# Kernel optimization log

Hardware: AMD Instinct MI355X
Metric: run time of the kernel (lower is better)

## Reference

```python
import jax, jax.numpy as jnp
import numpy as np

N = 30000
F_IN = 500
HID = 16
OUT = 3
E = 960000


def setup_inputs() -> dict:
    key = jax.random.key(0)
    ks = jax.random.split(key, 10)
    x = jax.random.normal(ks[0], (N, F_IN), dtype=jnp.float32)
    edge_index = jax.random.randint(ks[1], (2, E), 0, N, dtype=jnp.int32)
    # CNN params (torch Conv1d: weight [out, in, k], bias [out])
    s1 = 1.0 / np.sqrt(1 * 3)
    s2 = 1.0 / np.sqrt(HID * 3)
    conv1_w = jax.random.uniform(ks[2], (HID, 1, 3), jnp.float32, -s1, s1)
    conv1_b = jax.random.uniform(ks[3], (HID,), jnp.float32, -s1, s1)
    conv2_w = jax.random.uniform(ks[4], (HID, HID, 3), jnp.float32, -s2, s2)
    conv2_b = jax.random.uniform(ks[5], (HID,), jnp.float32, -s2, s2)
    # GCNConv params (glorot weight [in, out], zero bias)
    g1 = np.sqrt(6.0 / (HID + HID))
    g2 = np.sqrt(6.0 / (HID + OUT))
    gcn1_w = jax.random.uniform(ks[6], (HID, HID), jnp.float32, -g1, g1)
    gcn1_b = jnp.zeros((HID,), jnp.float32)
    gcn2_w = jax.random.uniform(ks[7], (HID, OUT), jnp.float32, -g2, g2)
    gcn2_b = jnp.zeros((OUT,), jnp.float32)
    return {"x": x, "conv1_w": conv1_w, "conv1_b": conv1_b,
            "conv2_w": conv2_w, "conv2_b": conv2_b,
            "gcn1_w": gcn1_w, "gcn1_b": gcn1_b,
            "gcn2_w": gcn2_w, "gcn2_b": gcn2_b,
            "edge_index": edge_index}


def _conv1d(x, w, b):
    # x: [N, C_in, L], w: [C_out, C_in, 3], padding=1
    y = jax.lax.conv_general_dilated(
        x, w, window_strides=(1,), padding=[(1, 1)],
        dimension_numbers=("NCH", "OIH", "NCH"))
    return y + b[None, :, None]


def _gcn_conv(x, w, b, src, dst, n):
    # x: [n, d_in] -> [n, d_out]; Kipf normalization with self-loops
    h = x @ w
    loop = jnp.arange(n, dtype=src.dtype)
    s = jnp.concatenate([src, loop])
    d = jnp.concatenate([dst, loop])
    deg = jax.ops.segment_sum(jnp.ones_like(d, dtype=h.dtype), d, num_segments=n)
    dinv = jnp.where(deg > 0, jax.lax.rsqrt(deg), 0.0)
    norm = dinv[s] * dinv[d]                      # [E+n]
    msg = h[s] * norm[:, None]                    # gather + scale
    return jax.ops.segment_sum(msg, d, num_segments=n) + b


def reference(x, conv1_w, conv1_b, conv2_w, conv2_b,
              gcn1_w, gcn1_b, gcn2_w, gcn2_b, edge_index):
    # CNN feature extractor over feature axis
    h = x[:, None, :]                             # [N, 1, F_IN]
    h = jax.nn.relu(_conv1d(h, conv1_w, conv1_b))  # [N, HID, F_IN]
    h = jax.nn.relu(_conv1d(h, conv2_w, conv2_b))  # [N, HID, F_IN]
    h = jnp.max(h, axis=2)                        # global max pool -> [N, HID]
    # GCN
    src, dst = edge_index[0], edge_index[1]
    n = h.shape[0]
    h = jax.nn.relu(_gcn_conv(h, gcn1_w, gcn1_b, src, dst, n))
    h = _gcn_conv(h, gcn2_w, gcn2_b, src, dst, n)  # [N, OUT]
    return jax.nn.log_softmax(h, axis=1)
```

## Files before the change

kernel.cpp:

```cpp
#include <hip/hip_runtime.h>
#include <hip/hip_bf16.h>

#define N_NODES 30000
#define F_INLEN 500
#define HID 16
#define OUTC 3
#define NEDGE 960000
#define YP 16
#define NBIN 938
#define HBLK 128
#define EPRH (NEDGE / HBLK)
#define ECAP 1536

typedef float  f32x4 __attribute__((ext_vector_type(4)));
typedef float  f32x2 __attribute__((ext_vector_type(2)));
typedef short  s16x8 __attribute__((ext_vector_type(8)));

static __device__ __forceinline__ unsigned short f2bf(float f) {
    unsigned int u = __float_as_uint(f);
    unsigned int r = (u + 0x7fffu + ((u >> 16) & 1u)) >> 16;
    return (unsigned short)r;
}
static __device__ __forceinline__ unsigned int pack_bf16x2(float v0, float v1) {
#if __has_builtin(__builtin_amdgcn_cvt_pk_bf16_f32)
    typedef __bf16 bf16x2_t __attribute__((ext_vector_type(2)));
    union { bf16x2_t v; unsigned int u; } cv;
    cv.v = __builtin_amdgcn_cvt_pk_bf16_f32(v0, v1);
    return cv.u;
#else
    return __builtin_amdgcn_perm(__float_as_uint(v1), __float_as_uint(v0), 0x07060302);
#endif
}

__global__ __launch_bounds__(256) void hist_kernel(
    const float* __restrict__ w2, short* __restrict__ bfragsG,
    const int* __restrict__ dst, int* __restrict__ degi, int* __restrict__ cntbase)
{
    const int tid = threadIdx.x;
    if (blockIdx.x == HBLK) {
        if (tid < 64) {
            const int n16 = tid & 15, q = tid >> 4;
#pragma unroll
            for (int j = 0; j < 8; j++) {
                {
                    const int c = q * 8 + j;
                    const int t = c >> 4, i = c & 15;
                    bfragsG[tid * 16 + j] = (short)f2bf(w2[n16 * 48 + i * 3 + t]);
                }
                {
                    const int c = 32 + q * 8 + j;
                    short v = 0;
                    if (c < 48) { const int t = c >> 4, i = c & 15; v = (short)f2bf(w2[n16 * 48 + i * 3 + t]); }
                    bfragsG[tid * 16 + 8 + j] = v;
                }
            }
        }
        return;
    }
    __shared__ int histH[NBIN];
    for (int i = tid; i < NBIN; i += 256) histH[i] = 0;
    __syncthreads();
    const int e0 = blockIdx.x * EPRH;
    for (int e = e0 + tid; e < e0 + EPRH; e += 256) {
        const int d = dst[e];
        atomicAdd(&histH[d >> 5], 1);
        atomicAdd(&degi[d], 1);
    }
    __syncthreads();
    for (int i = tid; i < NBIN; i += 256) cntbase[blockIdx.x * NBIN + i] = histH[i];
}

__global__ __launch_bounds__(256, 8) void conv_reorder(
    const float* __restrict__ x,
    const float* __restrict__ w1, const float* __restrict__ b1,
    const float* __restrict__ b2, const short* __restrict__ bfragsG,
    const int* __restrict__ src, const int* __restrict__ dst,
    const int* __restrict__ degi, const int* __restrict__ cntbase,
    int* __restrict__ packed, int* __restrict__ binstart,
    float* __restrict__ h0)
{
    __shared__ __align__(16) unsigned short yh[516 * YP];
    __shared__ __align__(16) float xp[502];
    __shared__ float red[64];

    const int tid = threadIdx.x;

    if (blockIdx.x < HBLK) {
        int* scA    = (int*)yh;
        int* scB    = scA + NBIN;
        int* totb   = scB + NBIN;
        int* cursor = totb + NBIN;
        const int blk = blockIdx.x;
        for (int bin = tid; bin < NBIN; bin += 256) {
            int tot = 0, psum = 0;
            for (int k = 0; k < HBLK; k++) {
                const int c = cntbase[k * NBIN + bin];
                tot += c;
                if (k < blk) psum += c;
            }
            scA[bin]    = tot;
            totb[bin]   = tot;
            cursor[bin] = psum;
        }
        __syncthreads();
        int* pA = scA; int* pB = scB;
        for (int off = 1; off < NBIN; off <<= 1) {
            for (int i = tid; i < NBIN; i += 256)
                pB[i] = pA[i] + ((i >= off) ? pA[i - off] : 0);
            __syncthreads();
            int* tp = pA; pA = pB; pB = tp;
        }
        for (int i = tid; i < NBIN; i += 256) {
            const int excl = pA[i] - totb[i];
            cursor[i] += excl;
            if (blk == 0) binstart[i] = excl;
        }
        if (blk == 0 && tid == 0) binstart[NBIN] = NEDGE;
        __syncthreads();
        const int e0 = blk * EPRH;
        for (int e = e0 + tid; e < e0 + EPRH; e += 256) {
            const int d = dst[e];
            const int pos = atomicAdd(&cursor[d >> 5], 1);
            packed[pos] = src[e] | (d << 15);
        }
        return;
    }

    const int node = blockIdx.x - HBLK;
    const int dgi  = degi[node];
    const int lane = tid & 63;
    const int wave = tid >> 6;
    const int n16  = lane & 15;
    const int q    = lane >> 4;

    if (tid == 0) { xp[0] = 0.f; xp[501] = 0.f; }
    if (tid < 125) {
        const float4 v = ((const float4*)(x + (long long)node * F_INLEN))[tid];
        xp[4 * tid + 1] = v.x; xp[4 * tid + 2] = v.y;
        xp[4 * tid + 3] = v.z; xp[4 * tid + 4] = v.w;
    }
    {
        const int ri = tid >> 4;
        const int row = (ri == 0) ? 0 : (500 + ri);
        yh[row * YP + (tid & 15)] = 0;
    }
    const s16x8* bfp = (const s16x8*)(bfragsG + lane * 16);
    const s16x8 bh0 = bfp[0], bh1 = bfp[1];

    f32x2 wt0[8], wt1[8], wt2[8], bbv[8];
#pragma unroll
    for (int cp = 0; cp < 8; cp++) {
        const int c0 = 2 * cp, c1 = 2 * cp + 1;
        wt0[cp] = (f32x2){w1[c0 * 3 + 0], w1[c1 * 3 + 0]};
        wt1[cp] = (f32x2){w1[c0 * 3 + 1], w1[c1 * 3 + 1]};
        wt2[cp] = (f32x2){w1[c0 * 3 + 2], w1[c1 * 3 + 2]};
        bbv[cp] = (f32x2){b1[c0], b1[c1]};
    }
    __syncthreads();

    for (int p = tid; p < 500; p += 256) {
        const float x0 = xp[p], x1 = xp[p + 1], x2 = xp[p + 2];
        const f32x2 xv0 = {x0, x0}, xv1 = {x1, x1}, xv2 = {x2, x2};
        const f32x2 zero = {0.f, 0.f};
        unsigned int hp[8];
#pragma unroll
        for (int cp = 0; cp < 8; cp++) {
            f32x2 a = __builtin_elementwise_fma(wt0[cp], xv0, bbv[cp]);
            a = __builtin_elementwise_fma(wt1[cp], xv1, a);
            a = __builtin_elementwise_fma(wt2[cp], xv2, a);
            a = __builtin_elementwise_max(a, zero);
            hp[cp] = pack_bf16x2(a[0], a[1]);
        }
        uint4* d = (uint4*)&yh[(p + 1) * YP];
        d[0] = make_uint4(hp[0], hp[1], hp[2], hp[3]);
        d[1] = make_uint4(hp[4], hp[5], hp[6], hp[7]);
    }
    __syncthreads();

    const unsigned short* ybase = yh + (n16 + (q >> 1)) * YP + (q & 1) * 8
                                     + wave * (8 * 16 * YP);
    f32x4 mxv = {-3.0e38f, -3.0e38f, -3.0e38f, -3.0e38f};
    f32x4 mxt = {-3.0e38f, -3.0e38f, -3.0e38f, -3.0e38f};
#pragma unroll
    for (int it = 0; it < 8; it++) {
        const s16x8 ah0 = *(const s16x8*)(ybase + it * (16 * YP));
        const s16x8 ah1 = *(const s16x8*)(ybase + it * (16 * YP) + 2 * YP);
        f32x4 acc = {0.f, 0.f, 0.f, 0.f};
        acc = __builtin_amdgcn_mfma_f32_16x16x32_bf16(ah0, bh0, acc, 0, 0, 0);
        acc = __builtin_amdgcn_mfma_f32_16x16x32_bf16(ah1, bh1, acc, 0, 0, 0);
        if (it < 7) mxv = __builtin_elementwise_max(mxv, acc);
        else        mxt = __builtin_elementwise_max(mxt, acc);
    }
    if (wave < 3 || q == 0) mxv = __builtin_elementwise_max(mxv, mxt);
    float m = fmaxf(fmaxf(mxv[0], mxv[1]), fmaxf(mxv[2], mxv[3]));
    m = fmaxf(m, __shfl_xor(m, 16));
    m = fmaxf(m, __shfl_xor(m, 32));
    if (lane < 16) red[wave * 16 + lane] = m;
    __syncthreads();
    if (tid < 16) {
        const float mm = fmaxf(fmaxf(red[tid], red[16 + tid]), fmaxf(red[32 + tid], red[48 + tid]));
        const float dv = rsqrtf((float)(dgi + 1));
        h0[node * HID + tid] = fmaxf(mm + b2[tid], 0.f) * dv;
    }
}

__global__ __launch_bounds__(512) void agg1_kernel(
    const int* __restrict__ binstart, int* __restrict__ packed,
    const float* __restrict__ h0, const int* __restrict__ degi,
    const float* __restrict__ W1, const float* __restrict__ b1g,
    const float* __restrict__ W2, float4* __restrict__ t2p4,
    int* __restrict__ binofs)
{
    __shared__ float w1s[256];
    __shared__ float w2s[48];
    __shared__ float b1s[16];
    __shared__ float accS[32 * 17];
    __shared__ int srt[ECAP];
    __shared__ int h32[32], ls32[32], lofs32[32];
    const int tid = threadIdx.x;
    const int blk = blockIdx.x;
    if (tid < 256) w1s[tid] = W1[tid];
    if (tid < 48) w2s[tid] = W2[tid];
    if (tid < 16) b1s[tid] = b1g[tid];
    if (tid < 32) {
        const int nd = blk * 32 + tid;
        const int v = (nd < N_NODES) ? degi[nd] : 0;
        h32[tid] = v;
        int inc = v;
#pragma unroll
        for (int off = 1; off < 32; off <<= 1) {
            const int y = __shfl_up(inc, off);
            if (tid >= off) inc += y;
        }
        ls32[tid] = inc - v;
        lofs32[tid] = inc - v;
    }
    const int beg = binstart[blk];
    const int cnt = binstart[blk + 1] - beg;
    __syncthreads();
    for (int j = tid; j < cnt; j += 512) {
        const int p = packed[beg + j];
        const int pos = atomicAdd(&lofs32[(p >> 15) & 31], 1);
        srt[pos] = p;
    }
    __syncthreads();
    for (int j = tid; j < cnt; j += 512) packed[beg + j] = srt[j];
    if (tid < 32) {
        binofs[blk * 64 + tid]      = ls32[tid];
        binofs[blk * 64 + 32 + tid] = h32[tid];
    }
    const int n = tid >> 4;
    const int eslot = (tid >> 2) & 3;
    const int q = tid & 3;
    const int node = blk * 32 + n;
    const bool valid = node < N_NODES;
    f32x4 acc = {0.f, 0.f, 0.f, 0.f};
    if (valid) {
        const int s0 = ls32[n];
        const int s1 = s0 + h32[n];
        for (int i = s0 + eslot; i < s1; i += 4) {
            const int s = srt[i] & 32767;
            acc += *(const f32x4*)(h0 + s * HID + q * 4);
        }
    }
#pragma unroll
    for (int c = 0; c < 4; c++) {
        acc[c] += __shfl_xor(acc[c], 4);
        acc[c] += __shfl_xor(acc[c], 8);
    }
    if (valid && eslot == 0) {
        acc += *(const f32x4*)(h0 + node * HID + q * 4);
        accS[n * 17 + q * 4 + 0] = acc[0];
        accS[n * 17 + q * 4 + 1] = acc[1];
        accS[n * 17 + q * 4 + 2] = acc[2];
        accS[n * 17 + q * 4 + 3] = acc[3];
    }
    __syncthreads();
    if (tid < 128) {
        const int n2 = tid >> 2;
        const int node2 = blk * 32 + n2;
        if (node2 < N_NODES) {
            const float dv = rsqrtf((float)(h32[n2] + 1));
            const int q2 = tid & 3;
            float y0 = 0.f, y1 = 0.f, y2 = 0.f, y3 = 0.f;
#pragma unroll
            for (int i = 0; i < 16; i++) {
                const float a = accS[n2 * 17 + i];
                y0 = fmaf(a, w1s[i * 16 + q2 * 4 + 0], y0);
                y1 = fmaf(a, w1s[i * 16 + q2 * 4 + 1], y1);
                y2 = fmaf(a, w1s[i * 16 + q2 * 4 + 2], y2);
                y3 = fmaf(a, w1s[i * 16 + q2 * 4 + 3], y3);
            }
            float d0 = 0.f, d1 = 0.f, d2 = 0.f;
            const float yv[4] = {y0, y1, y2, y3};
#pragma unroll
            for (int j = 0; j < 4; j++) {
                const int o = q2 * 4 + j;
                const float h = fmaxf(b1s[o] + dv * yv[j], 0.f);
                d0 = fmaf(h, w2s[o * 3 + 0], d0);
                d1 = fmaf(h, w2s[o * 3 + 1], d1);
                d2 = fmaf(h, w2s[o * 3 + 2], d2);
            }
            d0 += __shfl_xor(d0, 1); d0 += __shfl_xor(d0, 2);
            d1 += __shfl_xor(d1, 1); d1 += __shfl_xor(d1, 2);
            d2 += __shfl_xor(d2, 1); d2 += __shfl_xor(d2, 2);
            if (q2 == 0) t2p4[node2] = make_float4(d0 * dv, d1 * dv, d2 * dv, dv);
        }
    }
}

__global__ __launch_bounds__(512) void agg2_kernel(
    const int* __restrict__ binstart, const int* __restrict__ packed,
    const float4* __restrict__ t2p4, const int* __restrict__ binofs,
    const float* __restrict__ b2g, float* __restrict__ out)
{
    __shared__ int ofs[64];
    const int tid = threadIdx.x;
    const int blk = blockIdx.x;
    const int beg = binstart[blk];
    if (tid < 64) ofs[tid] = binofs[blk * 64 + tid];
    __syncthreads();
    const int n = tid >> 4;
    const int ln16 = tid & 15;
    const int node = blk * 32 + n;
    float a0 = 0.f, a1 = 0.f, a2 = 0.f;
    if (node < N_NODES) {
        const int s0 = ofs[n];
        const int s1 = s0 + ofs[32 + n];
        for (int i = s0 + ln16; i < s1; i += 16) {
            const int s = packed[beg + i] & 32767;
            const float4 v = t2p4[s];
            a0 += v.x; a1 += v.y; a2 += v.z;
        }
    }
#pragma unroll
    for (int msk = 1; msk < 16; msk <<= 1) {
        a0 += __shfl_xor(a0, msk);
        a1 += __shfl_xor(a1, msk);
        a2 += __shfl_xor(a2, msk);
    }
    if (ln16 == 0 && node < N_NODES) {
        const float4 self = t2p4[node];
        const float dv = self.w;
        const float z0 = b2g[0] + dv * (a0 + self.x);
        const float z1 = b2g[1] + dv * (a1 + self.y);
        const float z2 = b2g[2] + dv * (a2 + self.z);
        const float m = fmaxf(z0, fmaxf(z1, z2));
        const float lg = m + logf(expf(z0 - m) + expf(z1 - m) + expf(z2 - m));
        out[node * 3 + 0] = z0 - lg;
        out[node * 3 + 1] = z1 - lg;
        out[node * 3 + 2] = z2 - lg;
    }
}

extern "C" void kernel_launch(void* const* d_in, const int* in_sizes, int n_in,
                              void* d_out, int out_size, void* d_ws, size_t ws_size,
                              hipStream_t stream)
{
    const float* x   = (const float*)d_in[0];
    const float* w1  = (const float*)d_in[1];
    const float* b1  = (const float*)d_in[2];
    const float* w2  = (const float*)d_in[3];
    const float* b2  = (const float*)d_in[4];
    const float* g1w = (const float*)d_in[5];
    const float* g1b = (const float*)d_in[6];
    const float* g2w = (const float*)d_in[7];
    const float* g2b = (const float*)d_in[8];
    const int*   ei  = (const int*)d_in[9];
    const int* src = ei;
    const int* dst = ei + NEDGE;

    float* ws = (float*)d_ws;
    float*  h0      = ws;
    float4* t2p4    = (float4*)(ws + 480000);
    int*    degi    = (int*)(ws + 600000);
    int*    cntbase = (int*)(ws + 630000);
    int*    binstart= (int*)(ws + 750064);
    int*    packed  = (int*)(ws + 751104);
    int*    binofs  = (int*)(ws + 1711104);
    short*  bfragsG = (short*)(ws + 1771136);
    float*  out     = (float*)d_out;

    hipMemsetAsync(degi, 0, N_NODES * sizeof(int), stream);
    hist_kernel<<<HBLK + 1, 256, 0, stream>>>(w2, bfragsG, dst, degi, cntbase);
    conv_reorder<<<HBLK + N_NODES, 256, 0, stream>>>(x, w1, b1, b2, bfragsG,
                                                     src, dst, degi, cntbase,
                                                     packed, binstart, h0);
    agg1_kernel<<<NBIN, 512, 0, stream>>>(binstart, packed, h0, degi,
                                          g1w, g1b, g2w, t2p4, binofs);
    agg2_kernel<<<NBIN, 512, 0, stream>>>(binstart, packed, t2p4, binofs, g2b, out);
}
```

Measured before the change: 214.2 us.

## Replace bin prefix-scan with fixed-capacity bin slots and global atomic cursors

Drops the per-block shared histogram, the cntbase matrix and the 128-way prefix scan that computed exact bin start offsets. Each bin now gets a fixed slot of 1280 entries, filled through a global atomic cursor per bin, and the bin edge count is derived from the degree prefix inside agg1. This removes the scan work and the cntbase traffic but adds global atomic contention on 938 counters. It also assumes no bin ever holds more than 1280 edges, which holds only for roughly uniform random graphs.

```diff
diff --git a/kernel.cpp b/kernel.cpp
--- a/kernel.cpp
+++ b/kernel.cpp
@@ -10,6 +10,7 @@
 #define NBIN 938
 #define HBLK 128
 #define EPRH (NEDGE / HBLK)
+#define ECAPS 1280
 #define ECAP 1536
 
 typedef float  f32x4 __attribute__((ext_vector_type(4)));
@@ -34,7 +35,7 @@
 
 __global__ __launch_bounds__(256) void hist_kernel(
     const float* __restrict__ w2, short* __restrict__ bfragsG,
-    const int* __restrict__ dst, int* __restrict__ degi, int* __restrict__ cntbase)
+    const int* __restrict__ dst, int* __restrict__ degi)
 {
     const int tid = threadIdx.x;
     if (blockIdx.x == HBLK) {
@@ -57,17 +58,10 @@
         }
         return;
     }
-    __shared__ int histH[NBIN];
-    for (int i = tid; i < NBIN; i += 256) histH[i] = 0;
-    __syncthreads();
     const int e0 = blockIdx.x * EPRH;
     for (int e = e0 + tid; e < e0 + EPRH; e += 256) {
-        const int d = dst[e];
-        atomicAdd(&histH[d >> 5], 1);
-        atomicAdd(&degi[d], 1);
-    }
-    __syncthreads();
-    for (int i = tid; i < NBIN; i += 256) cntbase[blockIdx.x * NBIN + i] = histH[i];
+        atomicAdd(&degi[dst[e]], 1);
+    }
 }
 
 __global__ __launch_bounds__(256, 8) void conv_reorder(
@@ -75,9 +69,8 @@
     const float* __restrict__ w1, const float* __restrict__ b1,
     const float* __restrict__ b2, const short* __restrict__ bfragsG,
     const int* __restrict__ src, const int* __restrict__ dst,
-    const int* __restrict__ degi, const int* __restrict__ cntbase,
-    int* __restrict__ packed, int* __restrict__ binstart,
-    float* __restrict__ h0)
+    const int* __restrict__ degi, int* __restrict__ bincur,
+    int* __restrict__ packed, float* __restrict__ h0)
 {
     __shared__ __align__(16) unsigned short yh[516 * YP];
     __shared__ __align__(16) float xp[502];
@@ -86,42 +79,12 @@
     const int tid = threadIdx.x;
 
     if (blockIdx.x < HBLK) {
-        int* scA    = (int*)yh;
-        int* scB    = scA + NBIN;
-        int* totb   = scB + NBIN;
-        int* cursor = totb + NBIN;
-        const int blk = blockIdx.x;
-        for (int bin = tid; bin < NBIN; bin += 256) {
-            int tot = 0, psum = 0;
-            for (int k = 0; k < HBLK; k++) {
-                const int c = cntbase[k * NBIN + bin];
-                tot += c;
-                if (k < blk) psum += c;
-            }
-            scA[bin]    = tot;
-            totb[bin]   = tot;
-            cursor[bin] = psum;
-        }
-        __syncthreads();
-        int* pA = scA; int* pB = scB;
-        for (int off = 1; off < NBIN; off <<= 1) {
-            for (int i = tid; i < NBIN; i += 256)
-                pB[i] = pA[i] + ((i >= off) ? pA[i - off] : 0);
-            __syncthreads();
-            int* tp = pA; pA = pB; pB = tp;
-        }
-        for (int i = tid; i < NBIN; i += 256) {
-            const int excl = pA[i] - totb[i];
-            cursor[i] += excl;
-            if (blk == 0) binstart[i] = excl;
-        }
-        if (blk == 0 && tid == 0) binstart[NBIN] = NEDGE;
-        __syncthreads();
-        const int e0 = blk * EPRH;
+        const int e0 = blockIdx.x * EPRH;
         for (int e = e0 + tid; e < e0 + EPRH; e += 256) {
             const int d = dst[e];
-            const int pos = atomicAdd(&cursor[d >> 5], 1);
-            packed[pos] = src[e] | (d << 15);
+            const int b = d >> 5;
+            const int pos = atomicAdd(&bincur[b], 1);
+            packed[b * ECAPS + pos] = src[e] | (d << 15);
         }
         return;
     }
@@ -205,8 +168,8 @@
 }
 
 __global__ __launch_bounds__(512) void agg1_kernel(
-    const int* __restrict__ binstart, int* __restrict__ packed,
-    const float* __restrict__ h0, const int* __restrict__ degi,
+    int* __restrict__ packed, const float* __restrict__ h0,
+    const int* __restrict__ degi,
     const float* __restrict__ W1, const float* __restrict__ b1g,
     const float* __restrict__ W2, float4* __restrict__ t2p4,
     int* __restrict__ binofs)
@@ -235,9 +198,9 @@
         ls32[tid] = inc - v;
         lofs32[tid] = inc - v;
     }
-    const int beg = binstart[blk];
-    const int cnt = binstart[blk + 1] - beg;
-    __syncthreads();
+    const int beg = blk * ECAPS;
+    __syncthreads();
+    const int cnt = ls32[31] + h32[31];
     for (int j = tid; j < cnt; j += 512) {
         const int p = packed[beg + j];
         const int pos = atomicAdd(&lofs32[(p >> 15) & 31], 1);
@@ -310,14 +273,14 @@
 }
 
 __global__ __launch_bounds__(512) void agg2_kernel(
-    const int* __restrict__ binstart, const int* __restrict__ packed,
-    const float4* __restrict__ t2p4, const int* __restrict__ binofs,
-    const float* __restrict__ b2g, float* __restrict__ out)
+    const int* __restrict__ packed, const float4* __restrict__ t2p4,
+    const int* __restrict__ binofs, const float* __restrict__ b2g,
+    float* __restrict__ out)
 {
     __shared__ int ofs[64];
     const int tid = threadIdx.x;
     const int blk = blockIdx.x;
-    const int beg = binstart[blk];
+    const int beg = blk * ECAPS;
     if (tid < 64) ofs[tid] = binofs[blk * 64 + tid];
     __syncthreads();
     const int n = tid >> 4;
@@ -374,19 +337,18 @@
     float*  h0      = ws;
     float4* t2p4    = (float4*)(ws + 480000);
     int*    degi    = (int*)(ws + 600000);
-    int*    cntbase = (int*)(ws + 630000);
-    int*    binstart= (int*)(ws + 750064);
-    int*    packed  = (int*)(ws + 751104);
-    int*    binofs  = (int*)(ws + 1711104);
-    short*  bfragsG = (short*)(ws + 1771136);
+    int*    bincur  = (int*)(ws + 630000);
+    int*    packed  = (int*)(ws + 630960);
+    int*    binofs  = (int*)(ws + 1831600);
+    short*  bfragsG = (short*)(ws + 1891632);
     float*  out     = (float*)d_out;
 
-    hipMemsetAsync(degi, 0, N_NODES * sizeof(int), stream);
-    hist_kernel<<<HBLK + 1, 256, 0, stream>>>(w2, bfragsG, dst, degi, cntbase);
+    hipMemsetAsync(degi, 0, (N_NODES + 960) * sizeof(int), stream);
+    hist_kernel<<<HBLK + 1, 256, 0, stream>>>(w2, bfragsG, dst, degi);
     conv_reorder<<<HBLK + N_NODES, 256, 0, stream>>>(x, w1, b1, b2, bfragsG,
-                                                     src, dst, degi, cntbase,
-                                                     packed, binstart, h0);
-    agg1_kernel<<<NBIN, 512, 0, stream>>>(binstart, packed, h0, degi,
+                                                     src, dst, degi, bincur,
+                                                     packed, h0);
+    agg1_kernel<<<NBIN, 512, 0, stream>>>(packed, h0, degi,
                                           g1w, g1b, g2w, t2p4, binofs);
-    agg2_kernel<<<NBIN, 512, 0, stream>>>(binstart, packed, t2p4, binofs, g2b, out);
-}
+    agg2_kernel<<<NBIN, 512, 0, stream>>>(packed, t2p4, binofs, g2b, out);
+}
```

New measurement: 361.4 us. 68.7% more time.
